# Kernel tuning notes

Hardware: AMD Instinct MI355X
Metric: run time of the kernel (lower is better)

The kernel has to match this reference:

```python
import jax, jax.numpy as jnp
import numpy as np

N = 100000   # nodes per node type
E = 400000   # edges per relation
IN = 128     # input feature dim
HID = 128    # hidden_channels
H = 8        # heads
D = HID // H # head dim = 16
NEG_SLOPE = 0.2
BN_EPS = 1e-5


def setup_inputs() -> dict:
    key = jax.random.key(0)
    ks = jax.random.split(key, 24)
    f32 = jnp.float32
    def rn(k, shape, s):
        return jax.random.normal(k, shape, dtype=f32) * s
    inp = {
        'x_a': jax.random.normal(ks[0], (N, IN), dtype=f32),
        'x_b': jax.random.normal(ks[1], (N, IN), dtype=f32),
        'ei_ab': jax.random.randint(ks[2], (2, E), 0, N, dtype=jnp.int32),
        'ei_ba': jax.random.randint(ks[3], (2, E), 0, N, dtype=jnp.int32),
        'ei_aa': jax.random.randint(ks[4], (2, E), 0, N, dtype=jnp.int32),
        'ei_bb': jax.random.randint(ks[5], (2, E), 0, N, dtype=jnp.int32),
        # per-node-type projections (PyG Linear, with bias)
        'W_a': rn(ks[6], (IN, HID), 0.08), 'b_a': jnp.zeros((HID,), f32),
        'W_b': rn(ks[7], (IN, HID), 0.08), 'b_b': jnp.zeros((HID,), f32),
        # per-relation node-level attention vectors [H, D]
        'att_ab_s': rn(ks[8], (H, D), 0.2), 'att_ab_d': rn(ks[9], (H, D), 0.2),
        'att_ba_s': rn(ks[10], (H, D), 0.2), 'att_ba_d': rn(ks[11], (H, D), 0.2),
        'att_aa_s': rn(ks[12], (H, D), 0.2), 'att_aa_d': rn(ks[13], (H, D), 0.2),
        'att_bb_s': rn(ks[14], (H, D), 0.2), 'att_bb_d': rn(ks[15], (H, D), 0.2),
        # semantic-level attention: k_lin (Linear HID->HID) and query q
        'Wk': rn(ks[16], (HID, HID), 0.08), 'bk': jnp.zeros((HID,), f32),
        'q': rn(ks[17], (HID,), 0.2),
        # shared BatchNorm1d affine params
        'gamma': jnp.ones((HID,), f32), 'beta': jnp.zeros((HID,), f32),
    }
    return inp


def _edge_attn(h_src, h_dst, ei, att_s, att_d, n_dst):
    # GAT-style node-level attention for one relation (PyG HANConv message path)
    src, dst = ei[0], ei[1]
    a = (h_src * att_s).sum(-1)[src] + (h_dst * att_d).sum(-1)[dst]  # [E, H]
    a = jax.nn.leaky_relu(a, NEG_SLOPE)
    amax = jax.ops.segment_max(a, dst, num_segments=n_dst)            # [n_dst, H]
    amax = jnp.where(jnp.isfinite(amax), amax, 0.0)
    ex = jnp.exp(a - amax[dst])
    denom = jax.ops.segment_sum(ex, dst, num_segments=n_dst)[dst] + 1e-16
    w = ex / denom                                                    # segment softmax
    out = jax.ops.segment_sum(w[:, :, None] * h_src[src], dst, num_segments=n_dst)
    return jax.nn.relu(out.reshape(n_dst, H * D))                     # [n_dst, HID]


def _semantic(outs, Wk, bk, q):
    # semantic-level attention over relations targeting the same dst type
    st = jnp.stack(outs)                                   # [K, N, HID]
    score = (jnp.tanh(st @ Wk + bk).mean(axis=1) * q).sum(-1)  # [K]
    attn = jax.nn.softmax(score)
    return jnp.einsum('k,knf->nf', attn, st)


def _bn(x, gamma, beta):
    # BatchNorm1d in training mode: batch stats, biased variance
    mu = x.mean(axis=0)
    var = ((x - mu) ** 2).mean(axis=0)
    return (x - mu) * jax.lax.rsqrt(var + BN_EPS) * gamma + beta


def reference(x_a, x_b, ei_ab, ei_ba, ei_aa, ei_bb, W_a, b_a, W_b, b_b,
              att_ab_s, att_ab_d, att_ba_s, att_ba_d, att_aa_s, att_aa_d,
              att_bb_s, att_bb_d, Wk, bk, q, gamma, beta):
    h_a = (x_a @ W_a + b_a).reshape(N, H, D)
    h_b = (x_b @ W_b + b_b).reshape(N, H, D)
    o_ab = _edge_attn(h_a, h_b, ei_ab, att_ab_s, att_ab_d, N)  # dst b
    o_bb = _edge_attn(h_b, h_b, ei_bb, att_bb_s, att_bb_d, N)  # dst b
    o_ba = _edge_attn(h_b, h_a, ei_ba, att_ba_s, att_ba_d, N)  # dst a
    o_aa = _edge_attn(h_a, h_a, ei_aa, att_aa_s, att_aa_d, N)  # dst a
    out_a = _semantic([o_ba, o_aa], Wk, bk, q)
    out_b = _semantic([o_ab, o_bb], Wk, bk, q)
    return _bn(out_a, gamma, beta), _bn(out_b, gamma, beta)
```

## Files before the change

kernel.cpp:

```cpp
#include <hip/hip_runtime.h>

using u16 = unsigned short;
using u32 = unsigned int;
using bf16x8 = __attribute__((ext_vector_type(8))) short;
using f32x4  = __attribute__((ext_vector_type(4))) float;

__device__ __forceinline__ float bf2f(u16 v) { return __uint_as_float(((u32)v) << 16); }
__device__ __forceinline__ float blo(u32 u) { return __uint_as_float(u << 16); }
__device__ __forceinline__ float bhi(u32 u) { return __uint_as_float(u & 0xffff0000u); }
__device__ __forceinline__ u16 f2bf(float f) {
  u32 u = __float_as_uint(f);
  u += 0x7fffu + ((u >> 16) & 1u);
  return (u16)(u >> 16);
}
__device__ __forceinline__ float fast_tanh(float x) {
  float cx = fminf(fmaxf(x, -9.f), 9.f);
  float e = __expf(2.f * cx);
  return __fdividef(e - 1.f, e + 1.f);
}

__global__ __launch_bounds__(256) void prep_kernel(
    const float* __restrict__ Wa, const float* __restrict__ Wb,
    const float* __restrict__ Wk,
    u16* __restrict__ Ta, u16* __restrict__ Tb, u16* __restrict__ Tk,
    int* __restrict__ off, int M, float* __restrict__ zf, int ZF)
{
  const int bid = blockIdx.x, tid = threadIdx.x;
  if (bid < 192) {
    int w = bid >> 6, part = bid & 63;
    const float* W = (w == 0) ? Wa : (w == 1) ? Wb : Wk;
    u16* T = (w == 0) ? Ta : (w == 1) ? Tb : Tk;
    int idx = part * 256 + tid;
    int k = idx >> 7, n = idx & 127;
    T[n * 128 + k] = f2bf(W[idx]);
    return;
  }
  int zb = bid - 192;
  int Z = (M + 2047) / 2048;
  if (zb < Z) {
    int base = zb * 2048 + tid * 8;
#pragma unroll
    for (int j = 0; j < 8; ++j)
      if (base + j < M) off[base + j] = 0;
    return;
  }
  for (int i = tid; i < ZF; i += 256) zf[i] = 0.f;
}

__global__ __launch_bounds__(256) void fused1_kernel(
    const float* __restrict__ x_a, const float* __restrict__ x_b,
    const u16* __restrict__ WTa, const u16* __restrict__ WTb,
    const float* __restrict__ b_a, const float* __restrict__ b_b,
    const float* __restrict__ at0a, const float* __restrict__ at1a,
    const float* __restrict__ at2a, const float* __restrict__ at3a,
    const float* __restrict__ at0b, const float* __restrict__ at1b,
    const float* __restrict__ at2b, const float* __restrict__ at3b,
    u16* __restrict__ ha, u16* __restrict__ hb,
    float* __restrict__ a0a, float* __restrict__ a1a,
    float* __restrict__ a2a, float* __restrict__ a3a,
    float* __restrict__ a0b, float* __restrict__ a1b,
    float* __restrict__ a2b, float* __restrict__ a3b,
    const int* __restrict__ e0, const int* __restrict__ e1,
    const int* __restrict__ e2, const int* __restrict__ e3,
    int* __restrict__ cnt,
    int N, int E, int gproj, int nH)
{
  __shared__ __align__(16) u16 WTl[128 * 136];
  const int tid = threadIdx.x;
  const int bid = blockIdx.x;
  const int nP = 2 * gproj;
  const int tri = min(nP >> 1, nH);

  int role, idx;
  if (bid < 3 * tri) {
    int slot = bid % 3, grp = bid / 3;
    if (slot < 2) { role = 0; idx = grp * 2 + slot; }
    else          { role = 1; idx = grp; }
  } else {
    int rem = bid - 3 * tri;
    int pLeft = nP - 2 * tri;
    if (rem < pLeft) { role = 0; idx = 2 * tri + rem; }
    else             { role = 1; idx = tri + (rem - pLeft); }
  }

  if (role == 1) {
    const int r = idx & 3, ex = idx >> 2;
    const int* ei = (r == 0) ? e0 : (r == 1) ? e1 : (r == 2) ? e2 : e3;
    const int base = ex * 1024 + tid;
    int d[4];
#pragma unroll
    for (int j = 0; j < 4; ++j) {
      int e = base + j * 256;
      d[j] = (e < E) ? ei[E + e] : -1;
    }
#pragma unroll
    for (int j = 0; j < 4; ++j)
      if (d[j] >= 0) atomicAdd(&cnt[r * N + d[j]], 1);
    return;
  }

  const int ty = idx >= gproj;
  const int bx = idx - (ty ? gproj : 0);
  const float* x    = ty ? x_b : x_a;
  const u16*  WT    = ty ? WTb : WTa;
  const float* bias = ty ? b_b : b_a;
  const float* att0 = ty ? at0b : at0a;
  const float* att1 = ty ? at1b : at1a;
  const float* att2 = ty ? at2b : at2a;
  const float* att3 = ty ? at3b : at3a;
  u16* h_out = ty ? hb : ha;
  float* al0 = ty ? a0b : a0a;
  float* al1 = ty ? a1b : a1a;
  float* al2 = ty ? a2b : a2a;
  float* al3 = ty ? a3b : a3a;

  const uint4* Wg = (const uint4*)WT;
#pragma unroll
  for (int i = 0; i < 8; ++i) {
    int id = tid + 256 * i;
    uint4 v = Wg[id];
    int n = id >> 4, k8 = (id & 15) << 3;
    *(uint4*)&WTl[n * 136 + k8] = v;
  }
  __syncthreads();

  const int lane = tid & 63, wl = tid >> 6;
  const int col = lane & 15, g = lane >> 4;
  const int nb = bx * 64 + wl * 16;
  const int node = nb + col;
  const bool ok = node < N;

  const int arow = min(node, N - 1);
  const float* xr = x + (size_t)arow * 128;
  bf16x8 xh[4], xlo[4];
#pragma unroll
  for (int t = 0; t < 4; ++t) {
    float4 u = *(const float4*)&xr[t * 32 + g * 8];
    float4 v = *(const float4*)&xr[t * 32 + g * 8 + 4];
    float e[8] = {u.x, u.y, u.z, u.w, v.x, v.y, v.z, v.w};
    bf16x8 h8, l8;
#pragma unroll
    for (int j = 0; j < 8; ++j) {
      u16 hbt = (u16)(__float_as_uint(e[j]) >> 16);
      h8[j] = (short)hbt;
      l8[j] = (short)f2bf(e[j] - bf2f(hbt));
    }
    xh[t] = h8; xlo[t] = l8;
  }

  f32x4 acc[8];
#pragma unroll
  for (int c = 0; c < 8; ++c) {
    float4 bv = *(const float4*)&bias[c * 16 + g * 4];
    acc[c] = (f32x4){bv.x, bv.y, bv.z, bv.w};
  }

#pragma unroll
  for (int c = 0; c < 8; ++c) {
    const u16* wrow = &WTl[(c * 16 + col) * 136];
#pragma unroll
    for (int t = 0; t < 4; ++t) {
      bf16x8 wf = *(const bf16x8*)&wrow[t * 32 + g * 8];
      acc[c] = __builtin_amdgcn_mfma_f32_16x16x32_bf16(wf, xh[t],  acc[c], 0, 0, 0);
      acc[c] = __builtin_amdgcn_mfma_f32_16x16x32_bf16(wf, xlo[t], acc[c], 0, 0, 0);
    }
  }

  if (ok) {
#pragma unroll
    for (int c = 0; c < 8; ++c) {
      uint2 hv;
      hv.x = (u32)f2bf(acc[c][0]) | ((u32)f2bf(acc[c][1]) << 16);
      hv.y = (u32)f2bf(acc[c][2]) | ((u32)f2bf(acc[c][3]) << 16);
      *(uint2*)(h_out + (size_t)node * 128 + c * 16 + g * 4) = hv;
    }
  }

#pragma unroll
  for (int c = 0; c < 8; ++c) {
    float4 a0v = *(const float4*)&att0[c * 16 + g * 4];
    float4 a1v = *(const float4*)&att1[c * 16 + g * 4];
    float4 a2v = *(const float4*)&att2[c * 16 + g * 4];
    float4 a3v = *(const float4*)&att3[c * 16 + g * 4];
    float p0 = acc[c][0] * a0v.x + acc[c][1] * a0v.y + acc[c][2] * a0v.z + acc[c][3] * a0v.w;
    float p1 = acc[c][0] * a1v.x + acc[c][1] * a1v.y + acc[c][2] * a1v.z + acc[c][3] * a1v.w;
    float p2 = acc[c][0] * a2v.x + acc[c][1] * a2v.y + acc[c][2] * a2v.z + acc[c][3] * a2v.w;
    float p3 = acc[c][0] * a3v.x + acc[c][1] * a3v.y + acc[c][2] * a3v.z + acc[c][3] * a3v.w;
    p0 += __shfl_xor(p0, 16); p0 += __shfl_xor(p0, 32);
    p1 += __shfl_xor(p1, 16); p1 += __shfl_xor(p1, 32);
    p2 += __shfl_xor(p2, 16); p2 += __shfl_xor(p2, 32);
    p3 += __shfl_xor(p3, 16); p3 += __shfl_xor(p3, 32);
    if (ok && g == 0) {
      al0[node * 8 + c] = p0;
      al1[node * 8 + c] = p1;
      al2[node * 8 + c] = p2;
      al3[node * 8 + c] = p3;
    }
  }
}

__global__ __launch_bounds__(256) void scan1_kernel(int* __restrict__ data, int M,
                                                    int* __restrict__ bsum)
{
  __shared__ int ls[256];
  const int tid = threadIdx.x;
  const int base = blockIdx.x * 2048 + tid * 8;
  int v[8]; int s = 0;
#pragma unroll
  for (int j = 0; j < 8; ++j) v[j] = (base + j < M) ? data[base + j] : 0;
#pragma unroll
  for (int j = 0; j < 8; ++j) { int t = v[j]; v[j] = s; s += t; }
  ls[tid] = s;
  __syncthreads();
  for (int off = 1; off < 256; off <<= 1) {
    int t = (tid >= off) ? ls[tid - off] : 0;
    __syncthreads();
    ls[tid] += t;
    __syncthreads();
  }
  int texcl = ls[tid] - s;
#pragma unroll
  for (int j = 0; j < 8; ++j)
    if (base + j < M) data[base + j] = v[j] + texcl;
  if (tid == 255) bsum[blockIdx.x] = ls[255];
}

__global__ __launch_bounds__(256) void scan3_kernel(int* __restrict__ data,
                                                    const int* __restrict__ bsum, int M,
                                                    int* __restrict__ cursor)
{
  __shared__ int rs[4];
  const int tid = threadIdx.x;
  int v = (tid < (int)blockIdx.x) ? bsum[tid] : 0;
#pragma unroll
  for (int off = 32; off > 0; off >>= 1) v += __shfl_down(v, off);
  if ((tid & 63) == 0) rs[tid >> 6] = v;
  __syncthreads();
  const int add = rs[0] + rs[1] + rs[2] + rs[3];
  const int base = blockIdx.x * 2048 + tid * 8;
#pragma unroll
  for (int j = 0; j < 8; ++j) {
    int i = base + j;
    if (i < M) { int t = data[i] + add; data[i] = t; cursor[i] = t; }
  }
}

__global__ __launch_bounds__(256) void scatter_kernel(
    const int* __restrict__ e0, const int* __restrict__ e1,
    const int* __restrict__ e2, const int* __restrict__ e3,
    int E, int N, int* __restrict__ cursor, int* __restrict__ ssrc)
{
  const int r = blockIdx.y;
  const int* ei = (r == 0) ? e0 : (r == 1) ? e1 : (r == 2) ? e2 : e3;
  int e = blockIdx.x * 256 + threadIdx.x;
  if (e >= E) return;
  int s = ei[e], d = ei[E + e];
  int p = atomicAdd(&cursor[r * N + d], 1);
  ssrc[p] = s;
}

__global__ __launch_bounds__(256) void aggregate_kernel(
    const int* __restrict__ off, const int* __restrict__ ssrc,
    const float* __restrict__ aS0, const float* __restrict__ aS1,
    const float* __restrict__ aS2, const float* __restrict__ aS3,
    const float* __restrict__ aD0, const float* __restrict__ aD1,
    const float* __restrict__ aD2, const float* __restrict__ aD3,
    const u16* __restrict__ h0, const u16* __restrict__ h1,
    const u16* __restrict__ h2, const u16* __restrict__ h3,
    u32* __restrict__ o0, u32* __restrict__ o1,
    u32* __restrict__ o2, u32* __restrict__ o3,
    int N, int E)
{
  const int r = blockIdx.y;
  const float* aS = (r == 0) ? aS0 : (r == 1) ? aS1 : (r == 2) ? aS2 : aS3;
  const float* aD = (r == 0) ? aD0 : (r == 1) ? aD1 : (r == 2) ? aD2 : aD3;
  const u16*   h  = (r == 0) ? h0  : (r == 1) ? h1  : (r == 2) ? h2  : h3;
  u32*         o  = (r == 0) ? o0  : (r == 1) ? o1  : (r == 2) ? o2  : o3;

  const int wave = threadIdx.x >> 6, lane = threadIdx.x & 63;
  const int n = blockIdx.x * 4 + wave;
  if (n >= N) return;
  const int head = lane >> 3;
  const int hw = (lane >> 2) & 7;
  const int ew = lane & 3;
  const int srcb = head * 4;
  const int idx = r * N + n;
  const int p0 = off[idx];
  const int p1 = (idx + 1 < 4 * N) ? off[idx + 1] : 4 * E;
  const float aDw = aD[n * 8 + hw];
  const u32* h32 = (const u32*)h;

  float acc0 = 0.f, acc1 = 0.f, den = 0.f;
  int p = p0;
  for (; p + 4 <= p1; p += 4) {
    const int s0 = ssrc[p], s1 = ssrc[p + 1], s2 = ssrc[p + 2], s3 = ssrc[p + 3];
    const int sw = (ew & 1) ? ((ew & 2) ? s3 : s1) : ((ew & 2) ? s2 : s0);
    float lw = aS[sw * 8 + hw] + aDw;
    lw = fmaxf(lw, 0.2f * lw);
    const float wme = __expf(lw);
    const float w0 = __shfl(wme, srcb + 0);
    const float w1 = __shfl(wme, srcb + 1);
    const float w2 = __shfl(wme, srcb + 2);
    const float w3 = __shfl(wme, srcb + 3);
    const u32 v0 = h32[s0 * 64 + lane];
    const u32 v1 = h32[s1 * 64 + lane];
    const u32 v2 = h32[s2 * 64 + lane];
    const u32 v3 = h32[s3 * 64 + lane];
    den += (w0 + w1) + (w2 + w3);
    acc0 += w0 * blo(v0) + w1 * blo(v1) + w2 * blo(v2) + w3 * blo(v3);
    acc1 += w0 * bhi(v0) + w1 * bhi(v1) + w2 * bhi(v2) + w3 * bhi(v3);
  }
  const int rem = p1 - p;
  if (rem > 0) {
    const int s0 = ssrc[p];
    const int s1 = ssrc[(rem > 1) ? p + 1 : p];
    const int s2 = ssrc[(rem > 2) ? p + 2 : p];
    const int swi = (ew < rem) ? ew : 0;
    const int sw = (swi == 0) ? s0 : (swi == 1) ? s1 : s2;
    float lw = aS[sw * 8 + hw] + aDw;
    lw = fmaxf(lw, 0.2f * lw);
    const float wme = __expf(lw);
    const float w0 = __shfl(wme, srcb + 0);
    float w1 = __shfl(wme, srcb + 1);
    float w2 = __shfl(wme, srcb + 2);
    w1 = (rem > 1) ? w1 : 0.f;
    w2 = (rem > 2) ? w2 : 0.f;
    const u32 v0 = h32[s0 * 64 + lane];
    const u32 v1 = h32[s1 * 64 + lane];
    const u32 v2 = h32[s2 * 64 + lane];
    den += w0 + w1 + w2;
    acc0 += w0 * blo(v0) + w1 * blo(v1) + w2 * blo(v2);
    acc1 += w0 * bhi(v0) + w1 * bhi(v1) + w2 * bhi(v2);
  }
  const float inv = __fdividef(1.f, den + 1e-16f);
  const float r0 = fmaxf(acc0 * inv, 0.f);
  const float r1 = fmaxf(acc1 * inv, 0.f);
  o[n * 64 + lane] = (u32)f2bf(r0) | ((u32)f2bf(r1) << 16);
}

__global__ __launch_bounds__(256) void fused2_kernel(
    const u32* __restrict__ oba, const u32* __restrict__ oaa,
    const u32* __restrict__ oab, const u32* __restrict__ obb,
    const u16* __restrict__ WkT, const float* __restrict__ bk,
    const float* __restrict__ q, float* __restrict__ scores,
    float* __restrict__ sums_a, float* __restrict__ sums_b,
    int N, int R, int gproj)
{
  __shared__ __align__(16) u16 WTl[128 * 136];
  __shared__ float red[4];
  const int tid = threadIdx.x;
  const int bid = blockIdx.x;

  if (bid < 512) {
    const int t = bid >> 8, bx = bid & 255;
    const u32* p0 = t ? oab : oba;
    const u32* p1 = t ? obb : oaa;
    float* sums = t ? sums_b : sums_a;
    const int tc = tid & 31, tr = tid >> 5;
    float s0[4] = {0,0,0,0}, s1[4] = {0,0,0,0};
    float q00[4] = {0,0,0,0}, q11[4] = {0,0,0,0}, q01[4] = {0,0,0,0};
    const int rend = min((bx + 1) * R, N);
    for (int row = bx * R + tr; row < rend; row += 8) {
      uint2 v0 = *(const uint2*)&p0[row * 64 + tc * 2];
      uint2 v1 = *(const uint2*)&p1[row * 64 + tc * 2];
      float r0[4] = {blo(v0.x), bhi(v0.x), blo(v0.y), bhi(v0.y)};
      float r1[4] = {blo(v1.x), bhi(v1.x), blo(v1.y), bhi(v1.y)};
#pragma unroll
      for (int j = 0; j < 4; ++j) {
        s0[j] += r0[j]; s1[j] += r1[j];
        q00[j] += r0[j] * r0[j]; q11[j] += r1[j] * r1[j];
        q01[j] += r0[j] * r1[j];
      }
    }
    float* sm = (float*)WTl;
    for (int i = tid; i < 640; i += 256) sm[i] = 0.f;
    __syncthreads();
#pragma unroll
    for (int j = 0; j < 4; ++j) {
      int f = tc * 4 + j;
      atomicAdd(&sm[f], s0[j]);
      atomicAdd(&sm[128 + f], s1[j]);
      atomicAdd(&sm[256 + f], q00[j]);
      atomicAdd(&sm[384 + f], q11[j]);
      atomicAdd(&sm[512 + f], q01[j]);
    }
    __syncthreads();
    for (int i = tid; i < 640; i += 256) atomicAdd(&sums[i], sm[i]);
    return;
  }

  const int sid = bid - 512;
  const int rel = sid & 3, bx = sid >> 2;
  const u32* op = (rel == 0) ? oba : (rel == 1) ? oaa : (rel == 2) ? oab : obb;
  const u16* o = (const u16*)op;

  const uint4* Wg = (const uint4*)WkT;
#pragma unroll
  for (int i = 0; i < 8; ++i) {
    int id = tid + 256 * i;
    uint4 v = Wg[id];
    int n = id >> 4, k8 = (id & 15) << 3;
    *(uint4*)&WTl[n * 136 + k8] = v;
  }
  __syncthreads();

  const int lane = tid & 63, wl = tid >> 6;
  const int col = lane & 15, g = lane >> 4;
  const int nb = bx * 64 + wl * 16;

  float bv[8], qv[8];
#pragma unroll
  for (int c = 0; c < 8; ++c) {
    bv[c] = bk[c * 16 + col];
    qv[c] = q[c * 16 + col];
  }

  const int arow = min(nb + col, N - 1);
  const u16* orow = o + (size_t)arow * 128;
  bf16x8 af[4];
#pragma unroll
  for (int t = 0; t < 4; ++t) af[t] = *(const bf16x8*)&orow[t * 32 + g * 8];

  f32x4 acc[8];
#pragma unroll
  for (int c = 0; c < 8; ++c) acc[c] = (f32x4){bv[c], bv[c], bv[c], bv[c]};

#pragma unroll
  for (int c = 0; c < 8; ++c) {
    const u16* wrow = &WTl[(c * 16 + col) * 136];
#pragma unroll
    for (int t = 0; t < 4; ++t) {
      bf16x8 bf = *(const bf16x8*)&wrow[t * 32 + g * 8];
      acc[c] = __builtin_amdgcn_mfma_f32_16x16x32_bf16(af[t], bf, acc[c], 0, 0, 0);
    }
  }

  float p = 0.f;
  const int rowbase = nb + g * 4;
#pragma unroll
  for (int c = 0; c < 8; ++c) {
#pragma unroll
    for (int i = 0; i < 4; ++i) {
      int node = rowbase + i;
      if (node < N) p += fast_tanh(acc[c][i]) * qv[c];
    }
  }
#pragma unroll
  for (int off = 32; off > 0; off >>= 1) p += __shfl_down(p, off);
  if (lane == 0) red[wl] = p;
  __syncthreads();
  if (tid == 0) atomicAdd(&scores[rel], red[0] + red[1] + red[2] + red[3]);
}

__global__ __launch_bounds__(256) void bn_final_kernel(
    const u32* __restrict__ oba, const u32* __restrict__ oaa,
    const u32* __restrict__ oab, const u32* __restrict__ obb,
    const float* __restrict__ scores, const float* __restrict__ sums_a,
    const float* __restrict__ sums_b,
    const float* __restrict__ gamma, const float* __restrict__ beta,
    float* __restrict__ out, int N)
{
  const int t = blockIdx.y;
  const u32* o0 = t ? oab : oba;
  const u32* o1 = t ? obb : oaa;
  const float* sums = t ? sums_b : sums_a;
  float* op = out + (size_t)t * N * 128;

  const float invN = 1.f / (float)N;
  const float sc0 = scores[2 * t] * invN, sc1 = scores[2 * t + 1] * invN;
  const float m = fmaxf(sc0, sc1);
  const float e0 = expf(sc0 - m), e1 = expf(sc1 - m);
  const float einv = 1.f / (e0 + e1);
  const float a0 = e0 * einv, a1 = e1 * einv;

  __shared__ float scale[128], shift[128];
  if (threadIdx.x < 128) {
    int f = threadIdx.x;
    float S0 = sums[f], S1 = sums[128 + f];
    float Q00 = sums[256 + f], Q11 = sums[384 + f], Q01 = sums[512 + f];
    float mu = (a0 * S0 + a1 * S1) * invN;
    float msq = (a0 * a0 * Q00 + 2.f * a0 * a1 * Q01 + a1 * a1 * Q11) * invN;
    float var = fmaxf(msq - mu * mu, 0.f);
    float rs = rsqrtf(var + 1e-5f);
    float gm = gamma[f] * rs;
    scale[f] = gm;
    shift[f] = beta[f] - mu * gm;
  }
  __syncthreads();
  size_t total = (size_t)N * 128;
  for (size_t base = ((size_t)blockIdx.x * 256 + threadIdx.x) * 8; base < total;
       base += (size_t)gridDim.x * 2048) {
    int f0 = (int)(base & 127);
    uint4 p = *(const uint4*)&o0[base >> 1];
    uint4 q = *(const uint4*)&o1[base >> 1];
    float4 r0, r1;
    r0.x = (a0 * blo(p.x) + a1 * blo(q.x)) * scale[f0 + 0] + shift[f0 + 0];
    r0.y = (a0 * bhi(p.x) + a1 * bhi(q.x)) * scale[f0 + 1] + shift[f0 + 1];
    r0.z = (a0 * blo(p.y) + a1 * blo(q.y)) * scale[f0 + 2] + shift[f0 + 2];
    r0.w = (a0 * bhi(p.y) + a1 * bhi(q.y)) * scale[f0 + 3] + shift[f0 + 3];
    r1.x = (a0 * blo(p.z) + a1 * blo(q.z)) * scale[f0 + 4] + shift[f0 + 4];
    r1.y = (a0 * bhi(p.z) + a1 * bhi(q.z)) * scale[f0 + 5] + shift[f0 + 5];
    r1.z = (a0 * blo(p.w) + a1 * blo(q.w)) * scale[f0 + 6] + shift[f0 + 6];
    r1.w = (a0 * bhi(p.w) + a1 * bhi(q.w)) * scale[f0 + 7] + shift[f0 + 7];
    *(float4*)&op[base] = r0;
    *(float4*)&op[base + 4] = r1;
  }
}

extern "C" void kernel_launch(void* const* d_in, const int* in_sizes, int n_in,
                              void* d_out, int out_size, void* d_ws, size_t ws_size,
                              hipStream_t stream)
{
  const float* x_a      = (const float*)d_in[0];
  const float* x_b      = (const float*)d_in[1];
  const int* ei_ab      = (const int*)d_in[2];
  const int* ei_ba      = (const int*)d_in[3];
  const int* ei_aa      = (const int*)d_in[4];
  const int* ei_bb      = (const int*)d_in[5];
  const float* W_a      = (const float*)d_in[6];
  const float* b_a      = (const float*)d_in[7];
  const float* W_b      = (const float*)d_in[8];
  const float* b_b      = (const float*)d_in[9];
  const float* att_ab_s = (const float*)d_in[10];
  const float* att_ab_d = (const float*)d_in[11];
  const float* att_ba_s = (const float*)d_in[12];
  const float* att_ba_d = (const float*)d_in[13];
  const float* att_aa_s = (const float*)d_in[14];
  const float* att_aa_d = (const float*)d_in[15];
  const float* att_bb_s = (const float*)d_in[16];
  const float* att_bb_d = (const float*)d_in[17];
  const float* Wk       = (const float*)d_in[18];
  const float* bk       = (const float*)d_in[19];
  const float* q        = (const float*)d_in[20];
  const float* gamma    = (const float*)d_in[21];
  const float* beta     = (const float*)d_in[22];

  const int N = in_sizes[0] / 128;
  const int E = in_sizes[2] / 2;

  char* wp = (char*)d_ws;
  auto alloc = [&](size_t bytes) -> void* {
    void* p = (void*)wp;
    wp += (bytes + 255) & ~(size_t)255;
    return p;
  };
  u16* h_a = (u16*)alloc((size_t)N * 128 * 2);
  u16* h_b = (u16*)alloc((size_t)N * 128 * 2);
  float* A[8];
  for (int i = 0; i < 8; ++i) A[i] = (float*)alloc((size_t)N * 8 * 4);
  int* off    = (int*)alloc((size_t)4 * N * 4);
  int* cursor = (int*)alloc((size_t)4 * N * 4);
  int* bsum   = (int*)alloc(1024);
  int* ssrc   = (int*)alloc((size_t)4 * E * 4);
  u32* o_ab = (u32*)alloc((size_t)N * 64 * 4);
  u32* o_ba = (u32*)alloc((size_t)N * 64 * 4);
  u32* o_aa = (u32*)alloc((size_t)N * 64 * 4);
  u32* o_bb = (u32*)alloc((size_t)N * 64 * 4);
  float* scores = (float*)alloc(16);
  float* sums_a = (float*)alloc(2560);
  float* sums_b = (float*)alloc(2560);
  u16* WT_a = (u16*)alloc(128 * 128 * 2);
  u16* WT_b = (u16*)alloc(128 * 128 * 2);
  u16* WT_k = (u16*)alloc(128 * 128 * 2);
  if ((size_t)(wp - (char*)d_ws) > ws_size) return;

  const int M = 4 * N;
  const int Z = (M + 2047) / 2048;
  prep_kernel<<<192 + Z + 1, 256, 0, stream>>>(W_a, W_b, Wk, WT_a, WT_b, WT_k,
                                               off, M, scores, 1344);

  const int gproj = (N + 63) / 64;
  const int gEh = (E + 1023) / 1024;
  const int nH = 4 * gEh;
  const int g1total = 2 * gproj + nH;
  fused1_kernel<<<g1total, 256, 0, stream>>>(
      x_a, x_b, WT_a, WT_b, b_a, b_b,
      att_ab_s, att_aa_s, att_aa_d, att_ba_d,
      att_ab_d, att_bb_s, att_bb_d, att_ba_s,
      h_a, h_b,
      A[0], A[1], A[2], A[3], A[4], A[5], A[6], A[7],
      ei_ab, ei_ba, ei_aa, ei_bb,
      off, N, E, gproj, nH);

  const int G1 = (M + 2047) / 2048;
  scan1_kernel<<<G1, 256, 0, stream>>>(off, M, bsum);
  scan3_kernel<<<G1, 256, 0, stream>>>(off, bsum, M, cursor);
  const int gE = (E + 255) / 256;
  dim3 gsc(gE, 4);
  scatter_kernel<<<gsc, 256, 0, stream>>>(ei_ab, ei_ba, ei_aa, ei_bb, E, N, cursor, ssrc);

  dim3 gag((N + 3) / 4, 4);
  aggregate_kernel<<<gag, 256, 0, stream>>>(
      off, ssrc,
      A[0], A[7], A[1], A[5],
      A[4], A[3], A[2], A[6],
      h_a, h_b, h_a, h_b,
      o_ab, o_ba, o_aa, o_bb, N, E);

  const int R = (N + 255) / 256;
  const int g2total = 512 + 4 * gproj;
  fused2_kernel<<<g2total, 256, 0, stream>>>(
      o_ba, o_aa, o_ab, o_bb, WT_k, bk, q, scores, sums_a, sums_b, N, R, gproj);

  float* out = (float*)d_out;
  dim3 gbf(1024, 2);
  bn_final_kernel<<<gbf, 256, 0, stream>>>(o_ba, o_aa, o_ab, o_bb, scores,
                                           sums_a, sums_b, gamma, beta, out, N);
}
```

Before: 625.8 us.

## Fuse BatchNorm statistics accumulation into the aggregation kernel

The aggregation kernel now uses persistent grid-stride blocks, one grid row per destination node type. Each wave computes both incoming relations for a node and accumulates the per-feature sums and second moments needed for BatchNorm in registers, then reduces them through shared memory and global atomics. This removes the separate statistics pass in fused2 that re-read all four relation outputs. In exchange the aggregation grid becomes fixed-size and serialises the two relations per wave, which may reduce latency hiding for the irregular gathers.

Result: slower. 638.8 us (+2.1%).

```diff
diff --git a/kernel.cpp b/kernel.cpp
--- a/kernel.cpp
+++ b/kernel.cpp
@@ -259,37 +259,14 @@
   ssrc[p] = s;
 }
 
-__global__ __launch_bounds__(256) void aggregate_kernel(
+__device__ __forceinline__ u32 agg_rel(
     const int* __restrict__ off, const int* __restrict__ ssrc,
-    const float* __restrict__ aS0, const float* __restrict__ aS1,
-    const float* __restrict__ aS2, const float* __restrict__ aS3,
-    const float* __restrict__ aD0, const float* __restrict__ aD1,
-    const float* __restrict__ aD2, const float* __restrict__ aD3,
-    const u16* __restrict__ h0, const u16* __restrict__ h1,
-    const u16* __restrict__ h2, const u16* __restrict__ h3,
-    u32* __restrict__ o0, u32* __restrict__ o1,
-    u32* __restrict__ o2, u32* __restrict__ o3,
-    int N, int E)
-{
-  const int r = blockIdx.y;
-  const float* aS = (r == 0) ? aS0 : (r == 1) ? aS1 : (r == 2) ? aS2 : aS3;
-  const float* aD = (r == 0) ? aD0 : (r == 1) ? aD1 : (r == 2) ? aD2 : aD3;
-  const u16*   h  = (r == 0) ? h0  : (r == 1) ? h1  : (r == 2) ? h2  : h3;
-  u32*         o  = (r == 0) ? o0  : (r == 1) ? o1  : (r == 2) ? o2  : o3;
-
-  const int wave = threadIdx.x >> 6, lane = threadIdx.x & 63;
-  const int n = blockIdx.x * 4 + wave;
-  if (n >= N) return;
-  const int head = lane >> 3;
-  const int hw = (lane >> 2) & 7;
-  const int ew = lane & 3;
-  const int srcb = head * 4;
-  const int idx = r * N + n;
-  const int p0 = off[idx];
-  const int p1 = (idx + 1 < 4 * N) ? off[idx + 1] : 4 * E;
-  const float aDw = aD[n * 8 + hw];
-  const u32* h32 = (const u32*)h;
-
+    const float* __restrict__ aS, const float aDw,
+    const u32* __restrict__ h32, int ridxn, int N4, int E4,
+    int lane, int hw, int ew, int srcb, float& rf0, float& rf1)
+{
+  const int p0 = off[ridxn];
+  const int p1 = (ridxn + 1 < N4) ? off[ridxn + 1] : E4;
   float acc0 = 0.f, acc1 = 0.f, den = 0.f;
   int p = p0;
   for (; p + 4 <= p1; p += 4) {
@@ -335,62 +312,83 @@
   const float inv = __fdividef(1.f, den + 1e-16f);
   const float r0 = fmaxf(acc0 * inv, 0.f);
   const float r1 = fmaxf(acc1 * inv, 0.f);
-  o[n * 64 + lane] = (u32)f2bf(r0) | ((u32)f2bf(r1) << 16);
+  const u32 pk = (u32)f2bf(r0) | ((u32)f2bf(r1) << 16);
+  rf0 = blo(pk); rf1 = bhi(pk);
+  return pk;
+}
+
+__global__ __launch_bounds__(256) void aggregate_kernel(
+    const int* __restrict__ off, const int* __restrict__ ssrc,
+    const float* __restrict__ aS0, const float* __restrict__ aS1,
+    const float* __restrict__ aS2, const float* __restrict__ aS3,
+    const float* __restrict__ aD0, const float* __restrict__ aD1,
+    const float* __restrict__ aD2, const float* __restrict__ aD3,
+    const u16* __restrict__ h0, const u16* __restrict__ h1,
+    const u16* __restrict__ h2, const u16* __restrict__ h3,
+    u32* __restrict__ o0, u32* __restrict__ o1,
+    u32* __restrict__ o2, u32* __restrict__ o3,
+    float* __restrict__ sums_a, float* __restrict__ sums_b,
+    int N, int E, int BKS)
+{
+  __shared__ float sm[640];
+  const int t = blockIdx.y;
+  const int rX = t ? 0 : 1, rY = t ? 3 : 2;
+  const float* aSX = t ? aS0 : aS1;  const float* aDX = t ? aD0 : aD1;
+  const float* aSY = t ? aS3 : aS2;  const float* aDY = t ? aD3 : aD2;
+  const u32* hX = (const u32*)(t ? h0 : h1);
+  const u32* hY = (const u32*)(t ? h3 : h2);
+  u32* oX = t ? o0 : o1;
+  u32* oY = t ? o3 : o2;
+  float* sums = t ? sums_b : sums_a;
+
+  const int tid = threadIdx.x;
+  const int wave = tid >> 6, lane = tid & 63;
+  const int hw = (lane >> 2) & 7;
+  const int ew = lane & 3;
+  const int srcb = (lane >> 3) * 4;
+  const int N4 = 4 * N, E4 = 4 * E;
+  const int stride = BKS * 4;
+
+  for (int i = tid; i < 640; i += 256) sm[i] = 0.f;
+  __syncthreads();
+
+  float s0a = 0.f, s0b = 0.f, s1a = 0.f, s1b = 0.f;
+  float q00a = 0.f, q00b = 0.f, q11a = 0.f, q11b = 0.f, q01a = 0.f, q01b = 0.f;
+
+  for (int n = blockIdx.x * 4 + wave; n < N; n += stride) {
+    float xf0, xf1, yf0, yf1;
+    const u32 px = agg_rel(off, ssrc, aSX, aDX[n * 8 + hw], hX,
+                           rX * N + n, N4, E4, lane, hw, ew, srcb, xf0, xf1);
+    oX[n * 64 + lane] = px;
+    const u32 py = agg_rel(off, ssrc, aSY, aDY[n * 8 + hw], hY,
+                           rY * N + n, N4, E4, lane, hw, ew, srcb, yf0, yf1);
+    oY[n * 64 + lane] = py;
+    s0a += xf0; s0b += xf1; s1a += yf0; s1b += yf1;
+    q00a += xf0 * xf0; q00b += xf1 * xf1;
+    q11a += yf0 * yf0; q11b += yf1 * yf1;
+    q01a += xf0 * yf0; q01b += xf1 * yf1;
+  }
+
+  const int f0 = lane * 2, f1 = lane * 2 + 1;
+  atomicAdd(&sm[f0], s0a);        atomicAdd(&sm[f1], s0b);
+  atomicAdd(&sm[128 + f0], s1a);  atomicAdd(&sm[128 + f1], s1b);
+  atomicAdd(&sm[256 + f0], q00a); atomicAdd(&sm[256 + f1], q00b);
+  atomicAdd(&sm[384 + f0], q11a); atomicAdd(&sm[384 + f1], q11b);
+  atomicAdd(&sm[512 + f0], q01a); atomicAdd(&sm[512 + f1], q01b);
+  __syncthreads();
+  for (int i = tid; i < 640; i += 256) atomicAdd(&sums[i], sm[i]);
 }
 
 __global__ __launch_bounds__(256) void fused2_kernel(
     const u32* __restrict__ oba, const u32* __restrict__ oaa,
     const u32* __restrict__ oab, const u32* __restrict__ obb,
     const u16* __restrict__ WkT, const float* __restrict__ bk,
-    const float* __restrict__ q, float* __restrict__ scores,
-    float* __restrict__ sums_a, float* __restrict__ sums_b,
-    int N, int R, int gproj)
+    const float* __restrict__ q, float* __restrict__ scores, int N)
 {
   __shared__ __align__(16) u16 WTl[128 * 136];
   __shared__ float red[4];
   const int tid = threadIdx.x;
-  const int bid = blockIdx.x;
-
-  if (bid < 512) {
-    const int t = bid >> 8, bx = bid & 255;
-    const u32* p0 = t ? oab : oba;
-    const u32* p1 = t ? obb : oaa;
-    float* sums = t ? sums_b : sums_a;
-    const int tc = tid & 31, tr = tid >> 5;
-    float s0[4] = {0,0,0,0}, s1[4] = {0,0,0,0};
-    float q00[4] = {0,0,0,0}, q11[4] = {0,0,0,0}, q01[4] = {0,0,0,0};
-    const int rend = min((bx + 1) * R, N);
-    for (int row = bx * R + tr; row < rend; row += 8) {
-      uint2 v0 = *(const uint2*)&p0[row * 64 + tc * 2];
-      uint2 v1 = *(const uint2*)&p1[row * 64 + tc * 2];
-      float r0[4] = {blo(v0.x), bhi(v0.x), blo(v0.y), bhi(v0.y)};
-      float r1[4] = {blo(v1.x), bhi(v1.x), blo(v1.y), bhi(v1.y)};
-#pragma unroll
-      for (int j = 0; j < 4; ++j) {
-        s0[j] += r0[j]; s1[j] += r1[j];
-        q00[j] += r0[j] * r0[j]; q11[j] += r1[j] * r1[j];
-        q01[j] += r0[j] * r1[j];
-      }
-    }
-    float* sm = (float*)WTl;
-    for (int i = tid; i < 640; i += 256) sm[i] = 0.f;
-    __syncthreads();
-#pragma unroll
-    for (int j = 0; j < 4; ++j) {
-      int f = tc * 4 + j;
-      atomicAdd(&sm[f], s0[j]);
-      atomicAdd(&sm[128 + f], s1[j]);
-      atomicAdd(&sm[256 + f], q00[j]);
-      atomicAdd(&sm[384 + f], q11[j]);
-      atomicAdd(&sm[512 + f], q01[j]);
-    }
-    __syncthreads();
-    for (int i = tid; i < 640; i += 256) atomicAdd(&sums[i], sm[i]);
-    return;
-  }
-
-  const int sid = bid - 512;
-  const int rel = sid & 3, bx = sid >> 2;
+  const int rel = blockIdx.x & 3, bx = blockIdx.x >> 2;
   const u32* op = (rel == 0) ? oba : (rel == 1) ? oaa : (rel == 2) ? oab : obb;
   const u16* o = (const u16*)op;
 
@@ -589,18 +587,19 @@
   dim3 gsc(gE, 4);
   scatter_kernel<<<gsc, 256, 0, stream>>>(ei_ab, ei_ba, ei_aa, ei_bb, E, N, cursor, ssrc);
 
-  dim3 gag((N + 3) / 4, 4);
+  const int BKS = 1024;
+  dim3 gag(BKS, 2);
   aggregate_kernel<<<gag, 256, 0, stream>>>(
       off, ssrc,
       A[0], A[7], A[1], A[5],
       A[4], A[3], A[2], A[6],
       h_a, h_b, h_a, h_b,
-      o_ab, o_ba, o_aa, o_bb, N, E);
-
-  const int R = (N + 255) / 256;
-  const int g2total = 512 + 4 * gproj;
-  fused2_kernel<<<g2total, 256, 0, stream>>>(
-      o_ba, o_aa, o_ab, o_bb, WT_k, bk, q, scores, sums_a, sums_b, N, R, gproj);
+      o_ab, o_ba, o_aa, o_bb,
+      sums_a, sums_b, N, E, BKS);
+
+  dim3 g2(4 * gproj);
+  fused2_kernel<<<g2, 256, 0, stream>>>(
+      o_ba, o_aa, o_ab, o_bb, WT_k, bk, q, scores, N);
 
   float* out = (float*)d_out;
   dim3 gbf(1024, 2);
```
